# Kernel optimization log

Hardware: AMD Instinct MI355X
Metric: run time of the kernel (lower is better)

Reference implementation:

```python
import jax, jax.numpy as jnp
import numpy as np

N_NODES = 50000
N_EDGES = 1600000
D_IN = 128
D_HID = 128
D_OUT = 128


def setup_inputs() -> dict:
    key = jax.random.key(0)
    ks = jax.random.split(key, 12)
    s = 0.05
    return {
        "x": jax.random.normal(ks[0], (N_NODES, D_IN), jnp.float32),
        "src": jax.random.randint(ks[1], (N_EDGES,), 0, N_NODES),
        "dst": jax.random.randint(ks[2], (N_EDGES,), 0, N_NODES),
        "W_neigh1": jax.random.normal(ks[3], (D_HID, D_IN), jnp.float32) * s,
        "W_self1": jax.random.normal(ks[4], (D_HID, D_IN), jnp.float32) * s,
        "b_self1": jnp.zeros((D_HID,), jnp.float32),
        "W_neigh2": jax.random.normal(ks[5], (D_HID, D_HID), jnp.float32) * s,
        "W_self2": jax.random.normal(ks[6], (D_HID, D_HID), jnp.float32) * s,
        "b_self2": jnp.zeros((D_HID,), jnp.float32),
        "W_neigh3": jax.random.normal(ks[7], (D_OUT, D_HID), jnp.float32) * s,
        "W_self3": jax.random.normal(ks[8], (D_OUT, D_HID), jnp.float32) * s,
        "b_self3": jnp.zeros((D_OUT,), jnp.float32),
    }


def _sage_mean(h, src, dst, inv_deg, W_neigh, W_self, b_self):
    # DGL SAGEConv 'mean': fc_self(h) + fc_neigh(mean of in-neighbor feats)
    # zero in-degree nodes get zero neighbor term (inv_deg = 0 there is avoided
    # by clamping degree to >=1, sum is 0 anyway).
    neigh_sum = jax.ops.segment_sum(h[src], dst, num_segments=h.shape[0])  # [N, d]
    h_neigh = neigh_sum * inv_deg  # [N, d]
    return h @ W_self.T + b_self + h_neigh @ W_neigh.T


def reference(x, src, dst, W_neigh1, W_self1, b_self1, W_neigh2, W_self2, b_self2, W_neigh3, W_self3, b_self3):
    n = x.shape[0]
    deg = jax.ops.segment_sum(jnp.ones((src.shape[0],), x.dtype), dst, num_segments=n)
    inv_deg = (1.0 / jnp.maximum(deg, 1.0))[:, None]  # [N, 1]
    h = jax.nn.relu(_sage_mean(x, src, dst, inv_deg, W_neigh1, W_self1, b_self1))
    h = jax.nn.relu(_sage_mean(h, src, dst, inv_deg, W_neigh2, W_self2, b_self2))
    h = _sage_mean(h, src, dst, inv_deg, W_neigh3, W_self3, b_self3)
    return h
```

## Files before the change

### kernel.cpp

```cpp
#include <hip/hip_runtime.h>


constexpr int N_NODES = 50000;
constexpr int N_EDGES = 1600000;
constexpr int D = 128;
constexpr int SCAN_BLK = 1024;
constexpr int NCHUNK = (N_NODES + SCAN_BLK - 1) / SCAN_BLK;

typedef __bf16 bf16x8 __attribute__((ext_vector_type(8)));
typedef float f32x4 __attribute__((ext_vector_type(4)));
union U8 { bf16x8 v; __bf16 e[8]; };

__global__ void zero1(int* __restrict__ a, int n) {
    int i = blockIdx.x * blockDim.x + threadIdx.x;
    if (i < n) a[i] = 0;
}

__global__ void hist_pos(const int* __restrict__ dst, int* __restrict__ counts,
                         int* __restrict__ pos, int n) {
    int e = blockIdx.x * blockDim.x + threadIdx.x;
    if (e < n) pos[e] = atomicAdd(&counts[dst[e]], 1);
}

__global__ __launch_bounds__(SCAN_BLK) void scan_p1(const int* __restrict__ counts,
                                                    int* __restrict__ row_ptr,
                                                    float* __restrict__ inv_deg,
                                                    int* __restrict__ blocksums) {
    __shared__ int wsum[16];
    __shared__ int wpre[16];
    const int t = threadIdx.x;
    const int i = blockIdx.x * SCAN_BLK + t;
    const int lane = t & 63, w = t >> 6;
    int v = (i < N_NODES) ? counts[i] : 0;
    int x = v;
    #pragma unroll
    for (int off = 1; off < 64; off <<= 1) {
        int tt = __shfl_up(x, off, 64);
        if (lane >= off) x += tt;
    }
    if (lane == 63) wsum[w] = x;
    __syncthreads();
    if (t < 16) {
        int s = wsum[t];
        int y = s;
        #pragma unroll
        for (int off = 1; off < 16; off <<= 1) {
            int tt = __shfl_up(y, off, 64);
            if (t >= off) y += tt;
        }
        wpre[t] = y - s;
    }
    __syncthreads();
    if (i < N_NODES) {
        row_ptr[i] = wpre[w] + (x - v);
        inv_deg[i] = 1.0f / fmaxf((float)v, 1.0f);
    }
    if (t == SCAN_BLK - 1) blocksums[blockIdx.x] = wpre[15] + wsum[15];
}

__global__ void scan_p2(const int* __restrict__ blocksums, int* __restrict__ blockoffs) {
    const int t = threadIdx.x;
    int v = (t < NCHUNK) ? blocksums[t] : 0;
    int x = v;
    #pragma unroll
    for (int off = 1; off < 64; off <<= 1) {
        int tt = __shfl_up(x, off, 64);
        if (t >= off) x += tt;
    }
    if (t < NCHUNK) blockoffs[t] = x - v;
}

__global__ __launch_bounds__(SCAN_BLK) void scan_p3(int* __restrict__ row_ptr,
                                                    const int* __restrict__ blockoffs) {
    const int i = blockIdx.x * SCAN_BLK + threadIdx.x;
    if (i < N_NODES) row_ptr[i] += blockoffs[blockIdx.x];
    if (i == 0) row_ptr[N_NODES] = N_EDGES;
}

__global__ void scatter_edges(const int* __restrict__ src, const int* __restrict__ dst,
                              const int* __restrict__ pos, const int* __restrict__ row_ptr,
                              int* __restrict__ esrc, int n) {
    int e = blockIdx.x * blockDim.x + threadIdx.x;
    if (e < n) esrc[row_ptr[dst[e]] + pos[e]] = src[e];
}

__global__ void pack_w(const float* __restrict__ w0, const float* __restrict__ w1,
                       const float* __restrict__ w2, const float* __restrict__ w3,
                       const float* __restrict__ w4, const float* __restrict__ w5,
                       __bf16* __restrict__ outbase) {
    const float* ws[6] = {w0, w1, w2, w3, w4, w5};
    const float* W = ws[blockIdx.y];
    __bf16* o = outbase + (size_t)blockIdx.y * 32768;
    int idx = blockIdx.x * 256 + threadIdx.x;
    int t = idx & 7;
    int lane = (idx >> 3) & 63;
    int ks = (idx >> 9) & 3;
    int jt = idx >> 11;
    int j = jt * 16 + (lane & 15);
    int k = ks * 32 + (lane >> 4) * 8 + t;
    float w = W[j * D + k];
    __bf16 hi = (__bf16)w;
    o[idx] = hi;
    o[16384 + idx] = (__bf16)(w - (float)hi);
}

__global__ __launch_bounds__(256) void dual_gemm(
        const float* __restrict__ h, const __bf16* __restrict__ Bs,
        const __bf16* __restrict__ Bn, const float* __restrict__ bias,
        float* __restrict__ y_self, __bf16* __restrict__ z) {
    const int wave = threadIdx.x >> 6;
    const int lane = threadIdx.x & 63;
    const int tile = blockIdx.x * 4 + wave;
    if (tile >= N_NODES / 16) return;
    const int n0 = tile * 16;
    const int row = n0 + (lane & 15);
    const int koff = (lane >> 4) * 8;

    U8 ahi[4], alo[4];
    #pragma unroll
    for (int ks = 0; ks < 4; ++ks) {
        const float* p = h + (size_t)row * D + ks * 32 + koff;
        float f[8];
        *(f32x4*)&f[0] = *(const f32x4*)p;
        *(f32x4*)&f[4] = *(const f32x4*)(p + 4);
        #pragma unroll
        for (int t = 0; t < 8; ++t) {
            __bf16 hi = (__bf16)f[t];
            ahi[ks].e[t] = hi;
            alo[ks].e[t] = (__bf16)(f[t] - (float)hi);
        }
    }

    const int jcol = lane & 15;
    const int r0 = (lane >> 4) * 4;

    #pragma unroll 2
    for (int jt = 0; jt < 8; ++jt) {
        f32x4 accS = {0.f, 0.f, 0.f, 0.f};
        f32x4 accN = {0.f, 0.f, 0.f, 0.f};
        #pragma unroll
        for (int ks = 0; ks < 4; ++ks) {
            const size_t off = (((size_t)jt * 4 + ks) * 64 + lane) * 8;
            bf16x8 wsh = *(const bf16x8*)(Bs + off);
            bf16x8 wsl = *(const bf16x8*)(Bs + 16384 + off);
            bf16x8 wnh = *(const bf16x8*)(Bn + off);
            bf16x8 wnl = *(const bf16x8*)(Bn + 16384 + off);
            accS = __builtin_amdgcn_mfma_f32_16x16x32_bf16(ahi[ks].v, wsh, accS, 0, 0, 0);
            accS = __builtin_amdgcn_mfma_f32_16x16x32_bf16(alo[ks].v, wsh, accS, 0, 0, 0);
            accS = __builtin_amdgcn_mfma_f32_16x16x32_bf16(ahi[ks].v, wsl, accS, 0, 0, 0);
            accN = __builtin_amdgcn_mfma_f32_16x16x32_bf16(ahi[ks].v, wnh, accN, 0, 0, 0);
            accN = __builtin_amdgcn_mfma_f32_16x16x32_bf16(alo[ks].v, wnh, accN, 0, 0, 0);
            accN = __builtin_amdgcn_mfma_f32_16x16x32_bf16(ahi[ks].v, wnl, accN, 0, 0, 0);
        }
        const int j = jt * 16 + jcol;
        const float bj = bias[j];
        #pragma unroll
        for (int r = 0; r < 4; ++r) {
            const size_t n = n0 + r0 + r;
            y_self[n * D + j] = accS[r] + bj;
            z[n * D + j] = (__bf16)accN[r];
        }
    }
}

__global__ __launch_bounds__(256) void agg_add(
        const __bf16* __restrict__ z, const int* __restrict__ esrc,
        const int* __restrict__ row_ptr, const float* __restrict__ inv_deg,
        const float* __restrict__ y_self, float* __restrict__ out, int do_relu) {
    const int n = blockIdx.x * 4 + (threadIdx.x >> 6);
    const int lane = threadIdx.x & 63;
    const int s = lane >> 4;
    const int c = lane & 15;
    const int r0 = row_ptr[n], r1 = row_ptr[n + 1];

    float acc[8] = {0.f, 0.f, 0.f, 0.f, 0.f, 0.f, 0.f, 0.f};
    int e = r0 + s;
    for (; e + 12 < r1; e += 16) {
        int i0 = esrc[e], i1 = esrc[e + 4], i2 = esrc[e + 8], i3 = esrc[e + 12];
        U8 v0, v1, v2, v3;
        v0.v = *(const bf16x8*)(z + (size_t)i0 * D + c * 8);
        v1.v = *(const bf16x8*)(z + (size_t)i1 * D + c * 8);
        v2.v = *(const bf16x8*)(z + (size_t)i2 * D + c * 8);
        v3.v = *(const bf16x8*)(z + (size_t)i3 * D + c * 8);
        #pragma unroll
        for (int t = 0; t < 8; ++t)
            acc[t] += ((float)v0.e[t] + (float)v1.e[t]) + ((float)v2.e[t] + (float)v3.e[t]);
    }
    for (; e < r1; e += 4) {
        U8 v0;
        v0.v = *(const bf16x8*)(z + (size_t)esrc[e] * D + c * 8);
        #pragma unroll
        for (int t = 0; t < 8; ++t) acc[t] += (float)v0.e[t];
    }
    #pragma unroll
    for (int t = 0; t < 8; ++t) acc[t] += __shfl_down(acc[t], 32, 64);
    #pragma unroll
    for (int t = 0; t < 8; ++t) acc[t] += __shfl_down(acc[t], 16, 64);

    if (lane < 16) {
        const float idg = inv_deg[n];
        const float* yp = y_self + (size_t)n * D + c * 8;
        f32x4 y0 = *(const f32x4*)yp;
        f32x4 y1 = *(const f32x4*)(yp + 4);
        float o[8];
        #pragma unroll
        for (int t = 0; t < 4; ++t) o[t] = y0[t] + acc[t] * idg;
        #pragma unroll
        for (int t = 0; t < 4; ++t) o[4 + t] = y1[t] + acc[4 + t] * idg;
        if (do_relu) {
            #pragma unroll
            for (int t = 0; t < 8; ++t) o[t] = fmaxf(o[t], 0.f);
        }
        float* op = out + (size_t)n * D + c * 8;
        *(f32x4*)op = *(f32x4*)&o[0];
        *(f32x4*)(op + 4) = *(f32x4*)&o[4];
    }
}

extern "C" void kernel_launch(void* const* d_in, const int* in_sizes, int n_in,
                              void* d_out, int out_size, void* d_ws, size_t ws_size,
                              hipStream_t stream) {
    const float* x   = (const float*)d_in[0];
    const int* src   = (const int*)d_in[1];
    const int* dst   = (const int*)d_in[2];
    const float* Wn1 = (const float*)d_in[3];
    const float* Ws1 = (const float*)d_in[4];
    const float* b1  = (const float*)d_in[5];
    const float* Wn2 = (const float*)d_in[6];
    const float* Ws2 = (const float*)d_in[7];
    const float* b2  = (const float*)d_in[8];
    const float* Wn3 = (const float*)d_in[9];
    const float* Ws3 = (const float*)d_in[10];
    const float* b3  = (const float*)d_in[11];
    float* out = (float*)d_out;

    char* w = (char*)d_ws;
    float* inv_deg  = (float*)w;                w += 50176 * 4;
    int* counts     = (int*)w;                  w += 50176 * 4;
    int* row_ptr    = (int*)w;                  w += 50432 * 4;
    int* blocksums  = (int*)w;                  w += 64 * 4;
    int* blockoffs  = (int*)w;                  w += 64 * 4;
    int* esrc       = (int*)w;                  w += (size_t)N_EDGES * 4;
    __bf16* Bpk     = (__bf16*)w;               w += 6 * 32768 * 2;
    __bf16* zbuf    = (__bf16*)w;               w += (size_t)50176 * D * 2;
    float* bufA     = (float*)w;

    int* pos = (int*)zbuf;

    const __bf16* PWs1 = Bpk + 0 * 32768, *PWn1 = Bpk + 1 * 32768;
    const __bf16* PWs2 = Bpk + 2 * 32768, *PWn2 = Bpk + 3 * 32768;
    const __bf16* PWs3 = Bpk + 4 * 32768, *PWn3 = Bpk + 5 * 32768;

    zero1<<<(50176 + 255) / 256, 256, 0, stream>>>(counts, 50176);
    hist_pos<<<(N_EDGES + 511) / 512, 512, 0, stream>>>(dst, counts, pos, N_EDGES);
    scan_p1<<<NCHUNK, SCAN_BLK, 0, stream>>>(counts, row_ptr, inv_deg, blocksums);
    scan_p2<<<1, 64, 0, stream>>>(blocksums, blockoffs);
    scan_p3<<<NCHUNK, SCAN_BLK, 0, stream>>>(row_ptr, blockoffs);
    scatter_edges<<<(N_EDGES + 511) / 512, 512, 0, stream>>>(src, dst, pos, row_ptr,
                                                             esrc, N_EDGES);
    pack_w<<<dim3(64, 6), 256, 0, stream>>>(Ws1, Wn1, Ws2, Wn2, Ws3, Wn3, Bpk);

    const int ggrid = (N_NODES / 16 + 3) / 4;
    const int agrid = N_NODES / 4;

    dual_gemm<<<ggrid, 256, 0, stream>>>(x, PWs1, PWn1, b1, bufA, zbuf);
    agg_add<<<agrid, 256, 0, stream>>>(zbuf, esrc, row_ptr, inv_deg, bufA, bufA, 1);

    dual_gemm<<<ggrid, 256, 0, stream>>>(bufA, PWs2, PWn2, b2, out, zbuf);
    agg_add<<<agrid, 256, 0, stream>>>(zbuf, esrc, row_ptr, inv_deg, out, out, 1);

    dual_gemm<<<ggrid, 256, 0, stream>>>(out, PWs3, PWn3, b3, bufA, zbuf);
    agg_add<<<agrid, 256, 0, stream>>>(zbuf, esrc, row_ptr, inv_deg, bufA, out, 0);
}
```

Baseline: 435.0 us.

## Split neighbor features into column slabs so gathers hit smaller L2 working set

The GEMM now writes the bf16 neighbor projection in four 32-column slabs, each laid out node-major, instead of one row-major array. The aggregation kernel splits each node into four blocks, one per slab, with 16 edges in parallel per wave and 4 lanes per 64-byte row. The edge index loads use nontemporal hints. The intent is for each pass of random gathers to touch a 3.2MB slab that fits in cache rather than the full 12.8MB array. In exchange, the esrc and row_ptr reads are repeated four times, each gather is only 64 bytes, and more shuffle reductions are needed.

```diff
diff --git a/kernel.cpp b/kernel.cpp
--- a/kernel.cpp
+++ b/kernel.cpp
@@ -154,41 +154,44 @@
         }
         const int j = jt * 16 + jcol;
         const float bj = bias[j];
+        const size_t zslab = (size_t)(j >> 5) * N_NODES;
         #pragma unroll
         for (int r = 0; r < 4; ++r) {
             const size_t n = n0 + r0 + r;
             y_self[n * D + j] = accS[r] + bj;
-            z[n * D + j] = (__bf16)accN[r];
+            z[(zslab + n) * 32 + (j & 31)] = (__bf16)accN[r];
         }
     }
 }
 
 __global__ __launch_bounds__(256) void agg_add(
-        const __bf16* __restrict__ z, const int* __restrict__ esrc,
+        const __bf16* __restrict__ zq, const int* __restrict__ esrc,
         const int* __restrict__ row_ptr, const float* __restrict__ inv_deg,
         const float* __restrict__ y_self, float* __restrict__ out, int do_relu) {
-    const int n = blockIdx.x * 4 + (threadIdx.x >> 6);
+    const int q = blockIdx.x & 3;
+    const int grp = blockIdx.x >> 2;
+    const int n = grp * 4 + (threadIdx.x >> 6);
     const int lane = threadIdx.x & 63;
-    const int s = lane >> 4;
-    const int c = lane & 15;
+    const int slot = lane >> 2;
+    const int cl = lane & 3;
     const int r0 = row_ptr[n], r1 = row_ptr[n + 1];
+    const __bf16* zbase = zq + (size_t)q * N_NODES * 32 + cl * 8;
 
     float acc[8] = {0.f, 0.f, 0.f, 0.f, 0.f, 0.f, 0.f, 0.f};
-    int e = r0 + s;
-    for (; e + 12 < r1; e += 16) {
-        int i0 = esrc[e], i1 = esrc[e + 4], i2 = esrc[e + 8], i3 = esrc[e + 12];
-        U8 v0, v1, v2, v3;
-        v0.v = *(const bf16x8*)(z + (size_t)i0 * D + c * 8);
-        v1.v = *(const bf16x8*)(z + (size_t)i1 * D + c * 8);
-        v2.v = *(const bf16x8*)(z + (size_t)i2 * D + c * 8);
-        v3.v = *(const bf16x8*)(z + (size_t)i3 * D + c * 8);
-        #pragma unroll
-        for (int t = 0; t < 8; ++t)
-            acc[t] += ((float)v0.e[t] + (float)v1.e[t]) + ((float)v2.e[t] + (float)v3.e[t]);
-    }
-    for (; e < r1; e += 4) {
+    int e = r0 + slot;
+    for (; e + 16 < r1; e += 32) {
+        int i0 = __builtin_nontemporal_load(esrc + e);
+        int i1 = __builtin_nontemporal_load(esrc + e + 16);
+        U8 v0, v1;
+        v0.v = *(const bf16x8*)(zbase + (size_t)i0 * 32);
+        v1.v = *(const bf16x8*)(zbase + (size_t)i1 * 32);
+        #pragma unroll
+        for (int t = 0; t < 8; ++t) acc[t] += (float)v0.e[t] + (float)v1.e[t];
+    }
+    for (; e < r1; e += 16) {
+        int i0 = __builtin_nontemporal_load(esrc + e);
         U8 v0;
-        v0.v = *(const bf16x8*)(z + (size_t)esrc[e] * D + c * 8);
+        v0.v = *(const bf16x8*)(zbase + (size_t)i0 * 32);
         #pragma unroll
         for (int t = 0; t < 8; ++t) acc[t] += (float)v0.e[t];
     }
@@ -196,10 +199,14 @@
     for (int t = 0; t < 8; ++t) acc[t] += __shfl_down(acc[t], 32, 64);
     #pragma unroll
     for (int t = 0; t < 8; ++t) acc[t] += __shfl_down(acc[t], 16, 64);
-
-    if (lane < 16) {
+    #pragma unroll
+    for (int t = 0; t < 8; ++t) acc[t] += __shfl_down(acc[t], 8, 64);
+    #pragma unroll
+    for (int t = 0; t < 8; ++t) acc[t] += __shfl_down(acc[t], 4, 64);
+
+    if (lane < 4) {
         const float idg = inv_deg[n];
-        const float* yp = y_self + (size_t)n * D + c * 8;
+        const float* yp = y_self + (size_t)n * D + q * 32 + cl * 8;
         f32x4 y0 = *(const f32x4*)yp;
         f32x4 y1 = *(const f32x4*)(yp + 4);
         float o[8];
@@ -211,7 +218,7 @@
             #pragma unroll
             for (int t = 0; t < 8; ++t) o[t] = fmaxf(o[t], 0.f);
         }
-        float* op = out + (size_t)n * D + c * 8;
+        float* op = out + (size_t)n * D + q * 32 + cl * 8;
         *(f32x4*)op = *(f32x4*)&o[0];
         *(f32x4*)(op + 4) = *(f32x4*)&o[4];
     }
@@ -242,7 +249,7 @@
     int* blockoffs  = (int*)w;                  w += 64 * 4;
     int* esrc       = (int*)w;                  w += (size_t)N_EDGES * 4;
     __bf16* Bpk     = (__bf16*)w;               w += 6 * 32768 * 2;
-    __bf16* zbuf    = (__bf16*)w;               w += (size_t)50176 * D * 2;
+    __bf16* zbuf    = (__bf16*)w;               w += (size_t)N_NODES * D * 2;
     float* bufA     = (float*)w;
 
     int* pos = (int*)zbuf;
@@ -261,7 +268,7 @@
     pack_w<<<dim3(64, 6), 256, 0, stream>>>(Ws1, Wn1, Ws2, Wn2, Ws3, Wn3, Bpk);
 
     const int ggrid = (N_NODES / 16 + 3) / 4;
-    const int agrid = N_NODES / 4;
+    const int agrid = (N_NODES / 4) * 4;
 
     dual_gemm<<<ggrid, 256, 0, stream>>>(x, PWs1, PWn1, b1, bufA, zbuf);
     agg_add<<<agrid, 256, 0, stream>>>(zbuf, esrc, row_ptr, inv_deg, bufA, bufA, 1);
```

Result: slower. 553.9 us (+27.3%).
